# Optimization experiments

Measured on AMD Instinct MI355X. Metric: run time of the kernel, lower is better.

The kernel has to match this reference:

```python
import jax, jax.numpy as jnp
import numpy as np

N, E = 50000, 800000
IN_FEATS, HIDDEN, HEADS, NUM_CLASSES, EDGE_FEAT = 64, 64, 4, 4, 2
D_HEAD = HIDDEN // HEADS


def _lin(key, fan_in, fan_out):
    k1, k2 = jax.random.split(key)
    s = 1.0 / np.sqrt(fan_in)
    W = jax.random.uniform(k1, (fan_in, fan_out), jnp.float32, -s, s)
    b = jax.random.uniform(k2, (fan_out,), jnp.float32, -s, s)
    return W, b


def setup_inputs() -> dict:
    key = jax.random.key(0)
    ks = jax.random.split(key, 10)
    x = jax.random.normal(ks[0], (N, IN_FEATS), jnp.float32)
    edge_index = jax.random.randint(ks[1], (2, E), 0, N, jnp.int32)
    edge_attr = jax.random.normal(ks[2], (E, EDGE_FEAT), jnp.float32)
    Wn, bn = _lin(ks[3], IN_FEATS, HIDDEN)
    We, be = _lin(ks[4], EDGE_FEAT, HIDDEN)
    Wq, bq = _lin(ks[5], HIDDEN, HIDDEN)
    Wk, bk = _lin(ks[6], HIDDEN, HIDDEN)
    Wv, bv = _lin(ks[7], HIDDEN, HIDDEN)
    Ws, bs = _lin(ks[8], HIDDEN, HIDDEN)   # lin_skip (root weight)
    Wf, bf = _lin(ks[9], HIDDEN, NUM_CLASSES)
    return {"x": x, "edge_index": edge_index, "edge_attr": edge_attr,
            "Wn": Wn, "bn": bn, "We": We, "be": be,
            "Wq": Wq, "bq": bq, "Wk": Wk, "bk": bk, "Wv": Wv, "bv": bv,
            "Ws": Ws, "bs": bs, "Wf": Wf, "bf": bf}


def _segment_softmax(logits, seg, num_segments):
    # logits: [E, H], seg: [E] destination node ids
    m = jax.ops.segment_max(logits, seg, num_segments=num_segments)  # [N, H]
    m = jnp.where(jnp.isfinite(m), m, 0.0)
    e = jnp.exp(logits - m[seg])
    s = jax.ops.segment_sum(e, seg, num_segments=num_segments)
    return e / (s[seg] + 1e-16)


def reference(x, edge_index, edge_attr, Wn, bn, We, be, Wq, bq, Wk, bk, Wv, bv, Ws, bs, Wf, bf):
    src, dst = edge_index[0], edge_index[1]
    h = x @ Wn + bn                                   # [N, HIDDEN]
    ea = (edge_attr @ We + be).reshape(E, HEADS, D_HEAD)
    q = (h @ Wq + bq).reshape(N, HEADS, D_HEAD)
    k = (h @ Wk + bk).reshape(N, HEADS, D_HEAD)
    v = (h @ Wv + bv).reshape(N, HEADS, D_HEAD)
    # per-edge attention logits (PyG flow source_to_target: query at dst, key at src)
    logits = jnp.einsum('ehd,ehd->eh', q[dst], k[src]) / np.sqrt(D_HEAD)
    alpha = _segment_softmax(logits, dst, N)          # [E, H]
    # edge_attr added to values (lin_edge is None since edge_dim not set)
    msg = (v[src] + ea) * alpha[:, :, None]           # [E, H, D]
    out = jax.ops.segment_sum(msg, dst, num_segments=N).reshape(N, HIDDEN)
    out = out + h @ Ws + bs                           # root/skip connection
    # dropout is identity in eval mode
    edge_out = out[src] + out[dst]                    # [E, HIDDEN]
    return edge_out @ Wf + bf                         # [E, NUM_CLASSES]
```

## Files before the change

kernel.cpp:

```cpp
#include <hip/hip_runtime.h>
#include <hip/hip_bf16.h>
#include <hip/hip_fp16.h>

#define N_NODES 50000
#define N_EDGES 800000
#define NB_T64 ((N_NODES + 63) / 64)
#define WT_BLOCKS 16
#define CAP 64

#define BIN_SHIFT 8
#define NBINS ((N_NODES + 255) / 256)
#define CAP_BIN 5120
#define EPB 2048
#define NB_BIN ((N_EDGES + EPB - 1) / EPB)
#define NSEG 16

#define AGG_BLOCKS 2048
#define NGRP ((N_NODES + 15) / 16)

typedef unsigned short u16;
typedef unsigned int   u32;
typedef __attribute__((ext_vector_type(8))) short short8;
typedef __attribute__((ext_vector_type(8))) unsigned short ushort8;
typedef __attribute__((ext_vector_type(4))) float f32x4;

__device__ __forceinline__ float bf2f(u16 u) {
    union { u32 i; float f; } z; z.i = ((u32)u) << 16; return z.f;
}
__device__ __forceinline__ u16 f2bf(float f) {
    union { float f; u32 i; } z; z.f = f;
    u32 x = z.i;
    u32 r = (x + 0x7fffu + ((x >> 16) & 1u)) >> 16;
    return (u16)r;
}
__device__ __forceinline__ float h2f(u16 u) {
    __half h; *(u16*)&h = u; return __half2float(h);
}
__device__ __forceinline__ u16 f2h(float f) {
    __half h = __float2half_rn(f);
    return *(u16*)&h;
}
__device__ __forceinline__ float ldf(const void* p, size_t i, bool isbf) {
    return isbf ? bf2f(((const u16*)p)[i]) : ((const float*)p)[i];
}
__device__ __forceinline__ u16 ldbf(const void* p, size_t i, bool isbf) {
    return isbf ? ((const u16*)p)[i] : f2bf(((const float*)p)[i]);
}

#define WSB_COUNT 772

__global__ __launch_bounds__(256) void k_init(
    const void* __restrict__ Wn, const void* __restrict__ bn,
    const void* __restrict__ Wq, const void* __restrict__ bq,
    const void* __restrict__ Wk, const void* __restrict__ bk,
    const void* __restrict__ Wv, const void* __restrict__ bv,
    const void* __restrict__ Ws, const void* __restrict__ bs,
    const void* __restrict__ We, const void* __restrict__ be,
    const void* __restrict__ Wf, const void* __restrict__ bfv,
    const int* __restrict__ ei, const void* __restrict__ ea,
    u16* __restrict__ wsT, float* __restrict__ wsB,
    uint2* __restrict__ bins, u32* __restrict__ gcur,
    const int isbf)
{
    const int t = threadIdx.x, bid = blockIdx.x;
    if (bid >= WT_BLOCKS) {
        __shared__ u32 h[NBINS];
        __shared__ u32 off[NBINS];
        const int blk = bid - WT_BLOCKS;
        const int e0 = blk * EPB + t * 8;
        const bool vec = (e0 + 8 <= N_EDGES);
        int dv[8];
        if (vec) {
            const int4 a = *(const int4*)(ei + N_EDGES + e0);
            const int4 b = *(const int4*)(ei + N_EDGES + e0 + 4);
            dv[0] = a.x; dv[1] = a.y; dv[2] = a.z; dv[3] = a.w;
            dv[4] = b.x; dv[5] = b.y; dv[6] = b.z; dv[7] = b.w;
        } else {
            #pragma unroll
            for (int j = 0; j < 8; ++j)
                dv[j] = (e0 + j < N_EDGES) ? ei[N_EDGES + e0 + j] : -1;
        }
        if (t < NBINS) { h[t] = 0; off[t] = 0; }
        __syncthreads();
        #pragma unroll
        for (int j = 0; j < 8; ++j)
            if (dv[j] >= 0) atomicAdd(&h[dv[j] >> BIN_SHIFT], 1u);
        __syncthreads();
        if (t < NBINS && h[t] != 0) h[t] = atomicAdd(&gcur[t], h[t]);
        __syncthreads();
        int sv[8];
        if (vec) {
            const int4 a = *(const int4*)(ei + e0);
            const int4 b = *(const int4*)(ei + e0 + 4);
            sv[0] = a.x; sv[1] = a.y; sv[2] = a.z; sv[3] = a.w;
            sv[4] = b.x; sv[5] = b.y; sv[6] = b.z; sv[7] = b.w;
        } else {
            #pragma unroll
            for (int j = 0; j < 8; ++j)
                sv[j] = (e0 + j < N_EDGES) ? ei[e0 + j] : 0;
        }
        #pragma unroll
        for (int j = 0; j < 8; ++j) {
            if (dv[j] < 0) continue;
            const int e = e0 + j;
            float ea0, ea1;
            if (isbf) {
                const u32 w2 = ((const u32*)ea)[e];
                ea0 = bf2f((u16)(w2 & 0xffffu));
                ea1 = bf2f((u16)(w2 >> 16));
            } else {
                const float2 f2 = ((const float2*)ea)[e];
                ea0 = f2.x; ea1 = f2.y;
            }
            const __half2 hh = __floats2half2_rn(ea0, ea1);
            const int b = dv[j] >> BIN_SHIFT;
            const u32 rank = atomicAdd(&off[b], 1u);
            const u32 slot = h[b] + rank;
            if (slot < CAP_BIN) {
                uint2 r;
                r.x = (u32)sv[j] | ((u32)dv[j] << 16);
                r.y = *(const u32*)&hh;
                bins[(size_t)b * CAP_BIN + slot] = r;
            }
        }
        return;
    }

    const int i = bid * 256 + t;
    {
        const int kk = i >> 6, n = i & 63;
        const int o = n * 64 + kk;
        wsT[0 * 4096 + o] = ldbf(Wn, i, isbf);
        wsT[1 * 4096 + o] = ldbf(Wq, i, isbf);
        wsT[2 * 4096 + o] = ldbf(Wk, i, isbf);
        wsT[3 * 4096 + o] = ldbf(Wv, i, isbf);
        wsT[4 * 4096 + o] = ldbf(Ws, i, isbf);
    }
    if (bid == 0) {
        if (t < 64) {
            wsB[t]       = ldf(bn, t, isbf);
            wsB[64 + t]  = ldf(bq, t, isbf);
            wsB[128 + t] = ldf(bk, t, isbf);
            wsB[192 + t] = ldf(bv, t, isbf);
            wsB[256 + t] = ldf(bs, t, isbf);
            wsB[320 + t] = ldf(We, t, isbf);
            wsB[384 + t] = ldf(We, 64 + t, isbf);
            wsB[448 + t] = ldf(be, t, isbf);
        }
        wsB[512 + t] = ldf(Wf, t, isbf);
        if (t < 4) wsB[768 + t] = ldf(bfv, t, isbf);
    }
}

__global__ __launch_bounds__(512, 4) void k_bn(
    const void* __restrict__ x,
    const u16* __restrict__ wsT, const float* __restrict__ wsB,
    const uint2* __restrict__ bins, const u32* __restrict__ gcur,
    int* __restrict__ deg, uint2* __restrict__ rec,
    u16* __restrict__ qbf, u16* __restrict__ kvbf,
    u16* __restrict__ obf, const int isbf)
{
    __shared__ u16 xs[2 * 32 * 72];
    const int t = threadIdx.x, bid = blockIdx.x;

    if (bid < NBINS) {
        __shared__ u32 cnt2[(1 << BIN_SHIFT) * NSEG];
        const int lo = bid << BIN_SHIFT;
        for (int i = t; i < (1 << BIN_SHIFT) * NSEG; i += 512) cnt2[i] = 0;
        __syncthreads();
        int n = (int)gcur[bid];
        if (n > CAP_BIN) n = CAP_BIN;
        const uint2* bp = bins + (size_t)bid * CAP_BIN;
        for (int i = t; i < n; i += 512) {
            const uint2 r = bp[i];
            const u32 drel = (r.x >> 16) - (u32)lo;
            const u32 seg = (r.x & 0xffffu) >> 12;
            atomicAdd(&cnt2[drel * NSEG + seg], 1u);
        }
        __syncthreads();
        if (t < (1 << BIN_SHIFT)) {
            u32 s = 0;
            #pragma unroll
            for (int g2 = 0; g2 < NSEG; ++g2) {
                const u32 c = cnt2[t * NSEG + g2];
                cnt2[t * NSEG + g2] = s;
                s += c;
            }
            if (lo + t < N_NODES) deg[lo + t] = (int)s;
        }
        __syncthreads();
        for (int i = t; i < n; i += 512) {
            const uint2 r = bp[i];
            const u32 d = r.x >> 16;
            const u32 drel = d - (u32)lo;
            const u32 seg = (r.x & 0xffffu) >> 12;
            const u32 slot = atomicAdd(&cnt2[drel * NSEG + seg], 1u);
            if (slot < CAP) {
                uint2 o;
                o.x = r.x & 0xffffu;
                o.y = r.y;
                rec[((size_t)d << 6) + slot] = o;
            }
        }
        return;
    }

    const int tt = t & 255, half = t >> 8;
    const int w = tt >> 6, lane = tt & 63;
    const int l15 = lane & 15, quad = lane >> 4;
    const int base = (bid - NBINS) * 64 + half * 32;
    u16* xh = xs + half * (32 * 72);

    {
        const int m = tt >> 3, kc = tt & 7;
        const int node = base + m;
        short8 vd = {0, 0, 0, 0, 0, 0, 0, 0};
        if (node < N_NODES) {
            if (isbf) {
                vd = *(const short8*)((const u16*)x + (size_t)node * 64 + kc * 8);
            } else {
                const float4 f0 = *(const float4*)((const float*)x + (size_t)node * 64 + kc * 8);
                const float4 f1 = *(const float4*)((const float*)x + (size_t)node * 64 + kc * 8 + 4);
                vd[0] = f2bf(f0.x); vd[1] = f2bf(f0.y);
                vd[2] = f2bf(f0.z); vd[3] = f2bf(f0.w);
                vd[4] = f2bf(f1.x); vd[5] = f2bf(f1.y);
                vd[6] = f2bf(f1.z); vd[7] = f2bf(f1.w);
            }
        }
        *(short8*)(xh + m * 72 + kc * 8) = vd;
    }
    short8 b1[2][4];
    if (w < 2) {
        #pragma unroll
        for (int ks = 0; ks < 2; ++ks)
            #pragma unroll
            for (int nt = 0; nt < 4; ++nt)
                b1[ks][nt] = *(const short8*)(wsT + (nt * 16 + l15) * 64 + ks * 32 + quad * 8);
    }
    __syncthreads();

    if (w < 2) {
        f32x4 acc1[4];
        #pragma unroll
        for (int nt = 0; nt < 4; ++nt) acc1[nt] = (f32x4){0.f, 0.f, 0.f, 0.f};
        #pragma unroll
        for (int ks = 0; ks < 2; ++ks) {
            const short8 a = *(const short8*)(xh + (w * 16 + l15) * 72 + ks * 32 + quad * 8);
            #pragma unroll
            for (int nt = 0; nt < 4; ++nt)
                acc1[nt] = __builtin_amdgcn_mfma_f32_16x16x32_bf16(a, b1[ks][nt], acc1[nt], 0, 0, 0);
        }
        #pragma unroll
        for (int nt = 0; nt < 4; ++nt)
            #pragma unroll
            for (int r = 0; r < 4; ++r) {
                const int m = w * 16 + quad * 4 + r;
                const int col = nt * 16 + l15;
                xh[m * 72 + col] = f2bf(acc1[nt][r] + wsB[col]);
            }
    }
    short8 b2[2][4];
    {
        const u16* wt = wsT + (w + 1) * 4096;
        #pragma unroll
        for (int ks = 0; ks < 2; ++ks)
            #pragma unroll
            for (int nt = 0; nt < 4; ++nt)
                b2[ks][nt] = *(const short8*)(wt + (nt * 16 + l15) * 64 + ks * 32 + quad * 8);
    }
    __syncthreads();

    {
        f32x4 acc2[2][4];
        #pragma unroll
        for (int mt = 0; mt < 2; ++mt)
            #pragma unroll
            for (int nt = 0; nt < 4; ++nt) acc2[mt][nt] = (f32x4){0.f, 0.f, 0.f, 0.f};
        #pragma unroll
        for (int ks = 0; ks < 2; ++ks) {
            short8 a[2];
            #pragma unroll
            for (int mt = 0; mt < 2; ++mt)
                a[mt] = *(const short8*)(xh + (mt * 16 + l15) * 72 + ks * 32 + quad * 8);
            #pragma unroll
            for (int nt = 0; nt < 4; ++nt)
                #pragma unroll
                for (int mt = 0; mt < 2; ++mt)
                    acc2[mt][nt] = __builtin_amdgcn_mfma_f32_16x16x32_bf16(a[mt], b2[ks][nt], acc2[mt][nt], 0, 0, 0);
        }
        const float* bias = wsB + 64 + w * 64;
        #pragma unroll
        for (int mt = 0; mt < 2; ++mt)
            #pragma unroll
            for (int nt = 0; nt < 4; ++nt)
                #pragma unroll
                for (int r = 0; r < 4; ++r) {
                    const int node = base + mt * 16 + quad * 4 + r;
                    if (node >= N_NODES) continue;
                    const int col = nt * 16 + l15;
                    const float v = acc2[mt][nt][r] + bias[col];
                    if (w == 1) {
                        kvbf[(size_t)node * 128 + ((col >> 2) << 3) + (col & 3)] = f2h(v);
                    } else if (w == 2) {
                        kvbf[(size_t)node * 128 + ((col >> 2) << 3) + 4 + (col & 3)] = f2h(v);
                    } else if (w == 0) {
                        qbf[(size_t)node * 64 + col] = f2h(v);
                    } else {
                        obf[(size_t)node * 64 + col] = f2bf(v);
                    }
                }
    }
}

__global__ __launch_bounds__(256, 8) void k_agg(
    const int* __restrict__ deg,
    const uint2* __restrict__ rec,
    const u16* __restrict__ qbf, const u16* __restrict__ kvbf,
    const u16* __restrict__ obf,
    const float* __restrict__ wsB,
    float4* __restrict__ y)
{
    const int lane = threadIdx.x & 63;
    const int wave = threadIdx.x >> 6;
    const int sub = lane >> 4;
    const int lg  = lane & 15;

    const float4 we04 = *(const float4*)(wsB + 320 + lg * 4);
    const float4 we14 = *(const float4*)(wsB + 384 + lg * 4);
    const float4 bef4 = *(const float4*)(wsB + 448 + lg * 4);
    const float4 wf0 = *(const float4*)(wsB + 512 + (lg * 4 + 0) * 4);
    const float4 wf1 = *(const float4*)(wsB + 512 + (lg * 4 + 1) * 4);
    const float4 wf2 = *(const float4*)(wsB + 512 + (lg * 4 + 2) * 4);
    const float4 wf3 = *(const float4*)(wsB + 512 + (lg * 4 + 3) * 4);
    const u16* kvp = kvbf + lg * 8;

    for (int grp = blockIdx.x; grp < NGRP; grp += AGG_BLOCKS) {
        const int d = grp * 16 + wave * 4 + sub;
        if (d >= N_NODES) continue;

        const ushort4 q4u = *(const ushort4*)(qbf + (size_t)d * 64 + lg * 4);
        const float q0 = h2f(q4u.x), q1 = h2f(q4u.y);
        const float q2 = h2f(q4u.z), q3 = h2f(q4u.w);

        const int beg = d << 6;
        int dg = deg[d];
        dg = (dg > CAP) ? CAP : dg;

        float den = 0.f, sa0 = 0.f, sa1 = 0.f;
        float av0 = 0.f, av1 = 0.f, av2 = 0.f, av3 = 0.f;

        for (int j = 0; j < dg; j += 2) {
            const bool v1 = (j + 1) < dg;
            const uint2 r0 = rec[beg + j];
            const uint2 r1 = rec[beg + (v1 ? j + 1 : j)];
            const u32 rx1 = v1 ? r1.x : 0u;
            const ushort8 kva = *(const ushort8*)(kvp + (size_t)r0.x * 128);
            const ushort8 kvb = *(const ushort8*)(kvp + (size_t)rx1 * 128);
            float p0 =      h2f(kva[0]) * q0;
            p0 = fmaf(h2f(kva[1]), q1, p0);
            p0 = fmaf(h2f(kva[2]), q2, p0);
            p0 = fmaf(h2f(kva[3]), q3, p0);
            float p1 =      h2f(kvb[0]) * q0;
            p1 = fmaf(h2f(kvb[1]), q1, p1);
            p1 = fmaf(h2f(kvb[2]), q2, p1);
            p1 = fmaf(h2f(kvb[3]), q3, p1);
            p0 += __shfl_xor(p0, 1, 64);
            p1 += __shfl_xor(p1, 1, 64);
            p0 += __shfl_xor(p0, 2, 64);
            p1 += __shfl_xor(p1, 2, 64);
            const float ex0 = __expf(p0 * 0.25f);
            float ex1 = __expf(p1 * 0.25f);
            ex1 = v1 ? ex1 : 0.f;
            const u32 ry1 = v1 ? r1.y : 0u;
            den += ex0 + ex1;
            sa0 = fmaf(ex0, h2f((u16)(r0.y & 0xffffu)), sa0);
            sa1 = fmaf(ex0, h2f((u16)(r0.y >> 16)), sa1);
            sa0 = fmaf(ex1, h2f((u16)(ry1 & 0xffffu)), sa0);
            sa1 = fmaf(ex1, h2f((u16)(ry1 >> 16)), sa1);
            av0 = fmaf(ex0, h2f(kva[4]), av0);
            av1 = fmaf(ex0, h2f(kva[5]), av1);
            av2 = fmaf(ex0, h2f(kva[6]), av2);
            av3 = fmaf(ex0, h2f(kva[7]), av3);
            av0 = fmaf(ex1, h2f(kvb[4]), av0);
            av1 = fmaf(ex1, h2f(kvb[5]), av1);
            av2 = fmaf(ex1, h2f(kvb[6]), av2);
            av3 = fmaf(ex1, h2f(kvb[7]), av3);
        }

        const ushort4 o4 = *(const ushort4*)(obf + (size_t)d * 64 + lg * 4);
        const float rden = 1.0f / (den + 1e-16f);
        const float res0 = bf2f(o4.x) + (av0 + we04.x * sa0 + we14.x * sa1 + bef4.x * den) * rden;
        const float res1 = bf2f(o4.y) + (av1 + we04.y * sa0 + we14.y * sa1 + bef4.y * den) * rden;
        const float res2 = bf2f(o4.z) + (av2 + we04.z * sa0 + we14.z * sa1 + bef4.z * den) * rden;
        const float res3 = bf2f(o4.w) + (av3 + we04.w * sa0 + we14.w * sa1 + bef4.w * den) * rden;

        float y0 = res0 * wf0.x + res1 * wf1.x + res2 * wf2.x + res3 * wf3.x;
        float y1 = res0 * wf0.y + res1 * wf1.y + res2 * wf2.y + res3 * wf3.y;
        float y2 = res0 * wf0.z + res1 * wf1.z + res2 * wf2.z + res3 * wf3.z;
        float y3 = res0 * wf0.w + res1 * wf1.w + res2 * wf2.w + res3 * wf3.w;
        #pragma unroll
        for (int o = 1; o < 16; o <<= 1) {
            y0 += __shfl_xor(y0, o, 64);
            y1 += __shfl_xor(y1, o, 64);
            y2 += __shfl_xor(y2, o, 64);
            y3 += __shfl_xor(y3, o, 64);
        }
        if (lg == 0) {
            float4 yv;
            yv.x = y0 + 0.5f * wsB[768];
            yv.y = y1 + 0.5f * wsB[769];
            yv.z = y2 + 0.5f * wsB[770];
            yv.w = y3 + 0.5f * wsB[771];
            y[d] = yv;
        }
    }
}

__global__ __launch_bounds__(256) void k_edgeout(
    const int* __restrict__ ei,
    const float4* __restrict__ y,
    void* __restrict__ out, const int isbf)
{
    const int idx = blockIdx.x * 256 + threadIdx.x;
    const int e0 = idx * 2;
    if (e0 >= N_EDGES) return;
    const int2 ss = *(const int2*)(ei + e0);
    const int2 dd = *(const int2*)(ei + N_EDGES + e0);
    const float4 ya = y[ss.x], yb = y[dd.x];
    const float4 yc = y[ss.y], yd = y[dd.y];
    const float a0 = ya.x + yb.x, a1 = ya.y + yb.y;
    const float a2 = ya.z + yb.z, a3 = ya.w + yb.w;
    const float c0 = yc.x + yd.x, c1 = yc.y + yd.y;
    const float c2 = yc.z + yd.z, c3 = yc.w + yd.w;
    if (isbf) {
        uint4 r;
        r.x = (u32)f2bf(a0) | ((u32)f2bf(a1) << 16);
        r.y = (u32)f2bf(a2) | ((u32)f2bf(a3) << 16);
        r.z = (u32)f2bf(c0) | ((u32)f2bf(c1) << 16);
        r.w = (u32)f2bf(c2) | ((u32)f2bf(c3) << 16);
        *(uint4*)((u16*)out + (size_t)e0 * 4) = r;
    } else {
        float4 r0; r0.x = a0; r0.y = a1; r0.z = a2; r0.w = a3;
        float4 r1; r1.x = c0; r1.y = c1; r1.z = c2; r1.w = c3;
        *(float4*)((float*)out + (size_t)e0 * 4) = r0;
        *(float4*)((float*)out + (size_t)e0 * 4 + 4) = r1;
    }
}

extern "C" void kernel_launch(void* const* d_in, const int* in_sizes, int n_in,
                              void* d_out, int out_size, void* d_ws, size_t ws_size,
                              hipStream_t stream)
{
    (void)n_in; (void)out_size; (void)ws_size;
    const void* x   = d_in[0];
    const int*  ei  = (const int*)d_in[1];
    const void* ea  = d_in[2];
    const void* Wn  = d_in[3];  const void* bn  = d_in[4];
    const void* We  = d_in[5];  const void* be  = d_in[6];
    const void* Wq  = d_in[7];  const void* bq  = d_in[8];
    const void* Wk  = d_in[9];  const void* bk  = d_in[10];
    const void* Wv  = d_in[11]; const void* bv  = d_in[12];
    const void* Ws_ = d_in[13]; const void* bs  = d_in[14];
    const void* Wf  = d_in[15]; const void* bfv = d_in[16];

    const int isbf = (in_sizes[0] == N_NODES * 64 * 2) ? 1 : 0;

    char*   wsp   = (char*)d_ws;
    uint2*  rec   = (uint2*)wsp;
    float4* y     = (float4*)(rec + (size_t)N_NODES * CAP);
    u16*    qbf   = (u16*)(y + N_NODES);
    u16*    kvbf  = qbf + (size_t)N_NODES * 64;
    u16*    obf   = kvbf + (size_t)N_NODES * 128;
    u16*    wsT   = obf + (size_t)N_NODES * 64;
    float*  wsB   = (float*)(wsT + 5 * 4096);
    int*    deg   = (int*)(wsB + WSB_COUNT);
    uint2*  bins  = (uint2*)(deg + N_NODES);
    u32*    gcur  = (u32*)(bins + (size_t)NBINS * CAP_BIN);

    hipMemsetAsync(gcur, 0, NBINS * sizeof(u32), stream);
    k_init<<<WT_BLOCKS + NB_BIN, 256, 0, stream>>>(
        Wn, bn, Wq, bq, Wk, bk, Wv, bv, Ws_, bs, We, be, Wf, bfv, ei, ea,
        wsT, wsB, bins, gcur, isbf);
    k_bn<<<NBINS + NB_T64, 512, 0, stream>>>(x, wsT, wsB, bins, gcur,
                                             deg, rec, qbf, kvbf, obf, isbf);
    k_agg<<<AGG_BLOCKS, 256, 0, stream>>>(deg, rec, qbf, kvbf,
                                          obf, wsB, y);
    k_edgeout<<<(N_EDGES / 2 + 255) / 256, 256, 0, stream>>>(ei, y, d_out, isbf);
}
```

Measured before the change: 203.3 us.

## Store K/V gather table in FP8 and launch one aggregation block per node group

K and V node projections are now stored as 8-bit FP8 instead of FP16. The per-edge gather in the aggregation kernel therefore reads 8 bytes per lane instead of 16, and unpacks them with hardware packed FP8-to-FP32 conversions. The aggregation kernel also drops its grid-stride loop and launches one block per 16-node group. The aim is to halve the random-gather traffic that dominates aggregation, at the cost of much lower precision in the attention logits and values, which may break accuracy tolerance.

```diff
diff --git a/kernel.cpp b/kernel.cpp
--- a/kernel.cpp
+++ b/kernel.cpp
@@ -14,15 +14,14 @@
 #define EPB 2048
 #define NB_BIN ((N_EDGES + EPB - 1) / EPB)
 #define NSEG 16
-
-#define AGG_BLOCKS 2048
 #define NGRP ((N_NODES + 15) / 16)
 
 typedef unsigned short u16;
 typedef unsigned int   u32;
+typedef unsigned char  u8;
 typedef __attribute__((ext_vector_type(8))) short short8;
-typedef __attribute__((ext_vector_type(8))) unsigned short ushort8;
 typedef __attribute__((ext_vector_type(4))) float f32x4;
+typedef __attribute__((ext_vector_type(2))) float f32x2;
 
 __device__ __forceinline__ float bf2f(u16 u) {
     union { u32 i; float f; } z; z.i = ((u32)u) << 16; return z.f;
@@ -39,6 +38,10 @@
 __device__ __forceinline__ u16 f2h(float f) {
     __half h = __float2half_rn(f);
     return *(u16*)&h;
+}
+__device__ __forceinline__ u8 f2fp8(float f) {
+    const u32 p = (u32)__builtin_amdgcn_cvt_pk_fp8_f32(f, 0.f, 0, false);
+    return (u8)(p & 0xffu);
 }
 __device__ __forceinline__ float ldf(const void* p, size_t i, bool isbf) {
     return isbf ? bf2f(((const u16*)p)[i]) : ((const float*)p)[i];
@@ -157,7 +160,7 @@
     const u16* __restrict__ wsT, const float* __restrict__ wsB,
     const uint2* __restrict__ bins, const u32* __restrict__ gcur,
     int* __restrict__ deg, uint2* __restrict__ rec,
-    u16* __restrict__ qbf, u16* __restrict__ kvbf,
+    u16* __restrict__ qbf, u8* __restrict__ kvbf,
     u16* __restrict__ obf, const int isbf)
 {
     __shared__ u16 xs[2 * 32 * 72];
@@ -300,9 +303,9 @@
                     const int col = nt * 16 + l15;
                     const float v = acc2[mt][nt][r] + bias[col];
                     if (w == 1) {
-                        kvbf[(size_t)node * 128 + ((col >> 2) << 3) + (col & 3)] = f2h(v);
+                        kvbf[(size_t)node * 128 + ((col >> 2) << 3) + (col & 3)] = f2fp8(v);
                     } else if (w == 2) {
-                        kvbf[(size_t)node * 128 + ((col >> 2) << 3) + 4 + (col & 3)] = f2h(v);
+                        kvbf[(size_t)node * 128 + ((col >> 2) << 3) + 4 + (col & 3)] = f2fp8(v);
                     } else if (w == 0) {
                         qbf[(size_t)node * 64 + col] = f2h(v);
                     } else {
@@ -315,7 +318,7 @@
 __global__ __launch_bounds__(256, 8) void k_agg(
     const int* __restrict__ deg,
     const uint2* __restrict__ rec,
-    const u16* __restrict__ qbf, const u16* __restrict__ kvbf,
+    const u16* __restrict__ qbf, const u8* __restrict__ kvbf,
     const u16* __restrict__ obf,
     const float* __restrict__ wsB,
     float4* __restrict__ y)
@@ -324,95 +327,99 @@
     const int wave = threadIdx.x >> 6;
     const int sub = lane >> 4;
     const int lg  = lane & 15;
+    const int d = blockIdx.x * 16 + wave * 4 + sub;
+    if (d >= N_NODES) return;
+
+    const ushort4 q4u = *(const ushort4*)(qbf + (size_t)d * 64 + lg * 4);
+    const float q0 = h2f(q4u.x), q1 = h2f(q4u.y);
+    const float q2 = h2f(q4u.z), q3 = h2f(q4u.w);
+
+    const int beg = d << 6;
+    int dg = deg[d];
+    dg = (dg > CAP) ? CAP : dg;
+
+    float den = 0.f, sa0 = 0.f, sa1 = 0.f;
+    float av0 = 0.f, av1 = 0.f, av2 = 0.f, av3 = 0.f;
+
+    const u8* kvp = kvbf + lg * 8;
+    for (int j = 0; j < dg; j += 2) {
+        const bool v1 = (j + 1) < dg;
+        const uint2 r0 = rec[beg + j];
+        const uint2 r1 = rec[beg + (v1 ? j + 1 : j)];
+        const u32 rx1 = v1 ? r1.x : 0u;
+        const uint2 kva = *(const uint2*)(kvp + (size_t)r0.x * 128);
+        const uint2 kvb = *(const uint2*)(kvp + (size_t)rx1 * 128);
+        const f32x2 ka01 = __builtin_amdgcn_cvt_pk_f32_fp8((int)kva.x, false);
+        const f32x2 ka23 = __builtin_amdgcn_cvt_pk_f32_fp8((int)kva.x, true);
+        const f32x2 va01 = __builtin_amdgcn_cvt_pk_f32_fp8((int)kva.y, false);
+        const f32x2 va23 = __builtin_amdgcn_cvt_pk_f32_fp8((int)kva.y, true);
+        const f32x2 kb01 = __builtin_amdgcn_cvt_pk_f32_fp8((int)kvb.x, false);
+        const f32x2 kb23 = __builtin_amdgcn_cvt_pk_f32_fp8((int)kvb.x, true);
+        const f32x2 vb01 = __builtin_amdgcn_cvt_pk_f32_fp8((int)kvb.y, false);
+        const f32x2 vb23 = __builtin_amdgcn_cvt_pk_f32_fp8((int)kvb.y, true);
+        float p0 =      ka01.x * q0;
+        p0 = fmaf(ka01.y, q1, p0);
+        p0 = fmaf(ka23.x, q2, p0);
+        p0 = fmaf(ka23.y, q3, p0);
+        float p1 =      kb01.x * q0;
+        p1 = fmaf(kb01.y, q1, p1);
+        p1 = fmaf(kb23.x, q2, p1);
+        p1 = fmaf(kb23.y, q3, p1);
+        p0 += __shfl_xor(p0, 1, 64);
+        p1 += __shfl_xor(p1, 1, 64);
+        p0 += __shfl_xor(p0, 2, 64);
+        p1 += __shfl_xor(p1, 2, 64);
+        const float ex0 = __expf(p0 * 0.25f);
+        float ex1 = __expf(p1 * 0.25f);
+        ex1 = v1 ? ex1 : 0.f;
+        const u32 ry1 = v1 ? r1.y : 0u;
+        den += ex0 + ex1;
+        sa0 = fmaf(ex0, h2f((u16)(r0.y & 0xffffu)), sa0);
+        sa1 = fmaf(ex0, h2f((u16)(r0.y >> 16)), sa1);
+        sa0 = fmaf(ex1, h2f((u16)(ry1 & 0xffffu)), sa0);
+        sa1 = fmaf(ex1, h2f((u16)(ry1 >> 16)), sa1);
+        av0 = fmaf(ex0, va01.x, av0);
+        av1 = fmaf(ex0, va01.y, av1);
+        av2 = fmaf(ex0, va23.x, av2);
+        av3 = fmaf(ex0, va23.y, av3);
+        av0 = fmaf(ex1, vb01.x, av0);
+        av1 = fmaf(ex1, vb01.y, av1);
+        av2 = fmaf(ex1, vb23.x, av2);
+        av3 = fmaf(ex1, vb23.y, av3);
+    }
 
     const float4 we04 = *(const float4*)(wsB + 320 + lg * 4);
     const float4 we14 = *(const float4*)(wsB + 384 + lg * 4);
     const float4 bef4 = *(const float4*)(wsB + 448 + lg * 4);
+    const ushort4 o4 = *(const ushort4*)(obf + (size_t)d * 64 + lg * 4);
+    const float rden = 1.0f / (den + 1e-16f);
+    const float res0 = bf2f(o4.x) + (av0 + we04.x * sa0 + we14.x * sa1 + bef4.x * den) * rden;
+    const float res1 = bf2f(o4.y) + (av1 + we04.y * sa0 + we14.y * sa1 + bef4.y * den) * rden;
+    const float res2 = bf2f(o4.z) + (av2 + we04.z * sa0 + we14.z * sa1 + bef4.z * den) * rden;
+    const float res3 = bf2f(o4.w) + (av3 + we04.w * sa0 + we14.w * sa1 + bef4.w * den) * rden;
+
     const float4 wf0 = *(const float4*)(wsB + 512 + (lg * 4 + 0) * 4);
     const float4 wf1 = *(const float4*)(wsB + 512 + (lg * 4 + 1) * 4);
     const float4 wf2 = *(const float4*)(wsB + 512 + (lg * 4 + 2) * 4);
     const float4 wf3 = *(const float4*)(wsB + 512 + (lg * 4 + 3) * 4);
-    const u16* kvp = kvbf + lg * 8;
-
-    for (int grp = blockIdx.x; grp < NGRP; grp += AGG_BLOCKS) {
-        const int d = grp * 16 + wave * 4 + sub;
-        if (d >= N_NODES) continue;
-
-        const ushort4 q4u = *(const ushort4*)(qbf + (size_t)d * 64 + lg * 4);
-        const float q0 = h2f(q4u.x), q1 = h2f(q4u.y);
-        const float q2 = h2f(q4u.z), q3 = h2f(q4u.w);
-
-        const int beg = d << 6;
-        int dg = deg[d];
-        dg = (dg > CAP) ? CAP : dg;
-
-        float den = 0.f, sa0 = 0.f, sa1 = 0.f;
-        float av0 = 0.f, av1 = 0.f, av2 = 0.f, av3 = 0.f;
-
-        for (int j = 0; j < dg; j += 2) {
-            const bool v1 = (j + 1) < dg;
-            const uint2 r0 = rec[beg + j];
-            const uint2 r1 = rec[beg + (v1 ? j + 1 : j)];
-            const u32 rx1 = v1 ? r1.x : 0u;
-            const ushort8 kva = *(const ushort8*)(kvp + (size_t)r0.x * 128);
-            const ushort8 kvb = *(const ushort8*)(kvp + (size_t)rx1 * 128);
-            float p0 =      h2f(kva[0]) * q0;
-            p0 = fmaf(h2f(kva[1]), q1, p0);
-            p0 = fmaf(h2f(kva[2]), q2, p0);
-            p0 = fmaf(h2f(kva[3]), q3, p0);
-            float p1 =      h2f(kvb[0]) * q0;
-            p1 = fmaf(h2f(kvb[1]), q1, p1);
-            p1 = fmaf(h2f(kvb[2]), q2, p1);
-            p1 = fmaf(h2f(kvb[3]), q3, p1);
-            p0 += __shfl_xor(p0, 1, 64);
-            p1 += __shfl_xor(p1, 1, 64);
-            p0 += __shfl_xor(p0, 2, 64);
-            p1 += __shfl_xor(p1, 2, 64);
-            const float ex0 = __expf(p0 * 0.25f);
-            float ex1 = __expf(p1 * 0.25f);
-            ex1 = v1 ? ex1 : 0.f;
-            const u32 ry1 = v1 ? r1.y : 0u;
-            den += ex0 + ex1;
-            sa0 = fmaf(ex0, h2f((u16)(r0.y & 0xffffu)), sa0);
-            sa1 = fmaf(ex0, h2f((u16)(r0.y >> 16)), sa1);
-            sa0 = fmaf(ex1, h2f((u16)(ry1 & 0xffffu)), sa0);
-            sa1 = fmaf(ex1, h2f((u16)(ry1 >> 16)), sa1);
-            av0 = fmaf(ex0, h2f(kva[4]), av0);
-            av1 = fmaf(ex0, h2f(kva[5]), av1);
-            av2 = fmaf(ex0, h2f(kva[6]), av2);
-            av3 = fmaf(ex0, h2f(kva[7]), av3);
-            av0 = fmaf(ex1, h2f(kvb[4]), av0);
-            av1 = fmaf(ex1, h2f(kvb[5]), av1);
-            av2 = fmaf(ex1, h2f(kvb[6]), av2);
-            av3 = fmaf(ex1, h2f(kvb[7]), av3);
-        }
-
-        const ushort4 o4 = *(const ushort4*)(obf + (size_t)d * 64 + lg * 4);
-        const float rden = 1.0f / (den + 1e-16f);
-        const float res0 = bf2f(o4.x) + (av0 + we04.x * sa0 + we14.x * sa1 + bef4.x * den) * rden;
-        const float res1 = bf2f(o4.y) + (av1 + we04.y * sa0 + we14.y * sa1 + bef4.y * den) * rden;
-        const float res2 = bf2f(o4.z) + (av2 + we04.z * sa0 + we14.z * sa1 + bef4.z * den) * rden;
-        const float res3 = bf2f(o4.w) + (av3 + we04.w * sa0 + we14.w * sa1 + bef4.w * den) * rden;
-
-        float y0 = res0 * wf0.x + res1 * wf1.x + res2 * wf2.x + res3 * wf3.x;
-        float y1 = res0 * wf0.y + res1 * wf1.y + res2 * wf2.y + res3 * wf3.y;
-        float y2 = res0 * wf0.z + res1 * wf1.z + res2 * wf2.z + res3 * wf3.z;
-        float y3 = res0 * wf0.w + res1 * wf1.w + res2 * wf2.w + res3 * wf3.w;
-        #pragma unroll
-        for (int o = 1; o < 16; o <<= 1) {
-            y0 += __shfl_xor(y0, o, 64);
-            y1 += __shfl_xor(y1, o, 64);
-            y2 += __shfl_xor(y2, o, 64);
-            y3 += __shfl_xor(y3, o, 64);
-        }
-        if (lg == 0) {
-            float4 yv;
-            yv.x = y0 + 0.5f * wsB[768];
-            yv.y = y1 + 0.5f * wsB[769];
-            yv.z = y2 + 0.5f * wsB[770];
-            yv.w = y3 + 0.5f * wsB[771];
-            y[d] = yv;
-        }
+    float y0 = res0 * wf0.x + res1 * wf1.x + res2 * wf2.x + res3 * wf3.x;
+    float y1 = res0 * wf0.y + res1 * wf1.y + res2 * wf2.y + res3 * wf3.y;
+    float y2 = res0 * wf0.z + res1 * wf1.z + res2 * wf2.z + res3 * wf3.z;
+    float y3 = res0 * wf0.w + res1 * wf1.w + res2 * wf2.w + res3 * wf3.w;
+    #pragma unroll
+    for (int o = 1; o < 16; o <<= 1) {
+        y0 += __shfl_xor(y0, o, 64);
+        y1 += __shfl_xor(y1, o, 64);
+        y2 += __shfl_xor(y2, o, 64);
+        y3 += __shfl_xor(y3, o, 64);
+    }
+    if (lg == 0) {
+        float4 yv;
+        yv.x = y0 + 0.5f * wsB[768];
+        yv.y = y1 + 0.5f * wsB[769];
+        yv.z = y2 + 0.5f * wsB[770];
+        yv.w = y3 + 0.5f * wsB[771];
+        y[d] = yv;
     }
 }
 
@@ -469,8 +476,8 @@
     uint2*  rec   = (uint2*)wsp;
     float4* y     = (float4*)(rec + (size_t)N_NODES * CAP);
     u16*    qbf   = (u16*)(y + N_NODES);
-    u16*    kvbf  = qbf + (size_t)N_NODES * 64;
-    u16*    obf   = kvbf + (size_t)N_NODES * 128;
+    u8*     kvbf  = (u8*)(qbf + (size_t)N_NODES * 64);
+    u16*    obf   = (u16*)(kvbf + (size_t)N_NODES * 128);
     u16*    wsT   = obf + (size_t)N_NODES * 64;
     float*  wsB   = (float*)(wsT + 5 * 4096);
     int*    deg   = (int*)(wsB + WSB_COUNT);
@@ -483,7 +490,6 @@
         wsT, wsB, bins, gcur, isbf);
     k_bn<<<NBINS + NB_T64, 512, 0, stream>>>(x, wsT, wsB, bins, gcur,
                                              deg, rec, qbf, kvbf, obf, isbf);
-    k_agg<<<AGG_BLOCKS, 256, 0, stream>>>(deg, rec, qbf, kvbf,
-                                          obf, wsB, y);
+    k_agg<<<NGRP, 256, 0, stream>>>(deg, rec, qbf, kvbf, obf, wsB, y);
     k_edgeout<<<(N_EDGES / 2 + 255) / 256, 256, 0, stream>>>(ei, y, d_out, isbf);
 }
```

Result: faster. 188.2 us, median of 2 (-7.5%).
